# Kernel tuning notes

Hardware: AMD Instinct MI355X
Metric: run time of the kernel (lower is better)

The kernel has to match this reference:

```python
import jax, jax.numpy as jnp
import numpy as np

D_MODEL = 512
SCALE = 1.0 / (D_MODEL ** 0.5)  # module scales by 1/sqrt(d_model), not d_head
NEG = -1000000000.0

def setup_inputs() -> dict:
    key = jax.random.key(0)
    kq, kk, kv, kl = jax.random.split(key, 4)
    B, H, S, Dh = 4, 8, 2048, 64
    Q = jax.random.normal(kq, (B, H, S, Dh), dtype=jnp.float32)
    K = jax.random.normal(kk, (B, H, S, Dh), dtype=jnp.float32)
    V = jax.random.normal(kv, (B, H, S, Dh), dtype=jnp.float32)
    src_batch_lens = jax.random.randint(kl, (B,), 1, S + 1, dtype=jnp.int32)
    return {"Q": Q, "K": K, "V": V, "src_batch_lens": src_batch_lens}

def reference(Q, K, V, src_batch_lens):
    # scores: [B, H, Sq, Sk]
    scores = jnp.einsum('bhqd,bhkd->bhqk', Q, K) * SCALE
    Sk = K.shape[2]
    # mask keys at positions >= per-batch length
    key_mask = jnp.arange(Sk)[None, None, None, :] >= src_batch_lens[:, None, None, None]
    scores = jnp.where(key_mask, NEG, scores)
    attn = jax.nn.softmax(scores, axis=-1)
    # dropout is identity in eval/reference (p=0)
    context = jnp.einsum('bhqk,bhkd->bhqd', attn, V)
    return context
```

## Files before the change

kernel.cpp:

```cpp
#include <hip/hip_runtime.h>


#define S_LEN 2048
#define DH 64
#define QK_SCALE ((float)(1.4426950408889634 / 22.627416997969522))

typedef __attribute__((ext_vector_type(8))) short bf16x8;
typedef __attribute__((ext_vector_type(4))) float f32x4;

__device__ __forceinline__ short f2bf(float f) {
    __bf16 h = (__bf16)f;
    return __builtin_bit_cast(short, h);
}

#define SW(r, e) ((e) ^ (((r) & 7) << 3))

__global__ __launch_bounds__(256, 2)
void attn_fwd(const float* __restrict__ Qg, const float* __restrict__ Kg,
              const float* __restrict__ Vg, const int* __restrict__ lens,
              float* __restrict__ Og)
{
    __shared__ short Klds[2][64][64];
    __shared__ short Vt[2][64][64];

    const int tid  = threadIdx.x;
    const int wave = tid >> 6;
    const int lane = tid & 63;
    const int lr   = lane & 15;
    const int lg   = lane >> 4;

    const int bh = ((blockIdx.y & 3) << 3) | (blockIdx.y >> 2);
    const int L  = lens[bh >> 3];
    const int q0 = blockIdx.x * 64 + wave * 16;
    const size_t base = (size_t)bh * S_LEN * DH;

    bf16x8 qf[2];
    {
        const float* qrow = Qg + base + (size_t)(q0 + lr) * DH + 8 * lg;
        #pragma unroll
        for (int ks = 0; ks < 2; ++ks) {
            float4 a = *(const float4*)(qrow + 32 * ks);
            float4 b = *(const float4*)(qrow + 32 * ks + 4);
            bf16x8 f;
            f[0] = f2bf(a.x * QK_SCALE); f[1] = f2bf(a.y * QK_SCALE);
            f[2] = f2bf(a.z * QK_SCALE); f[3] = f2bf(a.w * QK_SCALE);
            f[4] = f2bf(b.x * QK_SCALE); f[5] = f2bf(b.y * QK_SCALE);
            f[6] = f2bf(b.z * QK_SCALE); f[7] = f2bf(b.w * QK_SCALE);
            qf[ks] = f;
        }
    }

    f32x4 Of[4];
    #pragma unroll
    for (int n = 0; n < 4; ++n) Of[n] = (f32x4){0.f, 0.f, 0.f, 0.f};
    f32x4 Dsum = (f32x4){0.f, 0.f, 0.f, 0.f};
    bf16x8 ones;
    #pragma unroll
    for (int j = 0; j < 8; ++j) ones[j] = (short)0x3F80;

    const int ntiles = (L + 63) >> 6;

    const int krow = tid >> 3;
    const int kc8  = (tid & 7) * 8;

    int vkey[16];
    #pragma unroll
    for (int i = 0; i < 16; ++i)
        vkey[i] = 16 * (wave & ~1) + (((i >> 2) & 1) << 4) + ((wave & 1) << 3)
                + ((i >> 3) << 2) + (i & 3);

    float4 kreg[4];
    float  vreg[16];

    {
        const float* kt = Kg + base;
        #pragma unroll
        for (int p = 0; p < 2; ++p) {
            kreg[2 * p]     = *(const float4*)(kt + (krow + 32 * p) * DH + kc8);
            kreg[2 * p + 1] = *(const float4*)(kt + (krow + 32 * p) * DH + kc8 + 4);
        }
        const float* vt = Vg + base;
        #pragma unroll
        for (int i = 0; i < 16; ++i)
            vreg[i] = vt[vkey[i] * DH + lane];
    }
    {
        #pragma unroll
        for (int p = 0; p < 2; ++p) {
            int row = krow + 32 * p;
            bf16x8 s;
            s[0] = f2bf(kreg[2*p].x); s[1] = f2bf(kreg[2*p].y);
            s[2] = f2bf(kreg[2*p].z); s[3] = f2bf(kreg[2*p].w);
            s[4] = f2bf(kreg[2*p+1].x); s[5] = f2bf(kreg[2*p+1].y);
            s[6] = f2bf(kreg[2*p+1].z); s[7] = f2bf(kreg[2*p+1].w);
            *(bf16x8*)&Klds[0][row][SW(row, kc8)] = s;
        }
        bf16x8 a, b;
        #pragma unroll
        for (int i = 0; i < 8; ++i) { a[i] = f2bf(vreg[i]); b[i] = f2bf(vreg[8 + i]); }
        *(bf16x8*)&Vt[0][lane][SW(lane, wave * 16)]     = a;
        *(bf16x8*)&Vt[0][lane][SW(lane, wave * 16 + 8)] = b;
    }
    __syncthreads();

    for (int t = 0; t < ntiles; ++t) {
        const int cur = t & 1;
        const int kb = t * 64;
        const bool pre = (t + 1 < ntiles);

        if (pre) {
            const float* kt = Kg + base + (size_t)(kb + 64) * DH;
            #pragma unroll
            for (int p = 0; p < 2; ++p) {
                kreg[2 * p]     = *(const float4*)(kt + (krow + 32 * p) * DH + kc8);
                kreg[2 * p + 1] = *(const float4*)(kt + (krow + 32 * p) * DH + kc8 + 4);
            }
            const float* vt = Vg + base + (size_t)(kb + 64) * DH;
            #pragma unroll
            for (int i = 0; i < 16; ++i)
                vreg[i] = vt[vkey[i] * DH + lane];
        }

        f32x4 Sv[4];
        #pragma unroll
        for (int n = 0; n < 4; ++n) Sv[n] = (f32x4){0.f, 0.f, 0.f, 0.f};
        #pragma unroll
        for (int ks = 0; ks < 2; ++ks) {
            #pragma unroll
            for (int n = 0; n < 4; ++n) {
                bf16x8 kf = *(const bf16x8*)&Klds[cur][16 * n + lr][SW(16 * n + lr, 8 * lg + 32 * ks)];
                Sv[n] = __builtin_amdgcn_mfma_f32_16x16x32_bf16(kf, qf[ks], Sv[n], 0, 0, 0);
            }
        }

        if (kb + 64 > L) {
            #pragma unroll
            for (int n = 0; n < 4; ++n) {
                const int kbase = kb + 16 * n + 4 * lg;
                #pragma unroll
                for (int r = 0; r < 4; ++r)
                    if (kbase + r >= L) Sv[n][r] = -1e30f;
            }
        }

        bf16x8 pf[2];
        #pragma unroll
        for (int ks = 0; ks < 2; ++ks) {
            #pragma unroll
            for (int h = 0; h < 2; ++h) {
                #pragma unroll
                for (int r = 0; r < 4; ++r)
                    pf[ks][4 * h + r] = f2bf(exp2f(Sv[2 * ks + h][r]));
            }
        }

        #pragma unroll
        for (int ks = 0; ks < 2; ++ks) {
            Dsum = __builtin_amdgcn_mfma_f32_16x16x32_bf16(pf[ks], ones, Dsum, 0, 0, 0);
            #pragma unroll
            for (int n = 0; n < 4; ++n) {
                bf16x8 vf = *(const bf16x8*)&Vt[cur][16 * n + lr][SW(16 * n + lr, 8 * lg + 32 * ks)];
                Of[n] = __builtin_amdgcn_mfma_f32_16x16x32_bf16(pf[ks], vf, Of[n], 0, 0, 0);
            }
        }

        if (pre) {
            const int b = cur ^ 1;
            #pragma unroll
            for (int p = 0; p < 2; ++p) {
                int row = krow + 32 * p;
                bf16x8 s;
                s[0] = f2bf(kreg[2*p].x); s[1] = f2bf(kreg[2*p].y);
                s[2] = f2bf(kreg[2*p].z); s[3] = f2bf(kreg[2*p].w);
                s[4] = f2bf(kreg[2*p+1].x); s[5] = f2bf(kreg[2*p+1].y);
                s[6] = f2bf(kreg[2*p+1].z); s[7] = f2bf(kreg[2*p+1].w);
                *(bf16x8*)&Klds[b][row][SW(row, kc8)] = s;
            }
            bf16x8 a, bb;
            #pragma unroll
            for (int i = 0; i < 8; ++i) { a[i] = f2bf(vreg[i]); bb[i] = f2bf(vreg[8 + i]); }
            *(bf16x8*)&Vt[b][lane][SW(lane, wave * 16)]     = a;
            *(bf16x8*)&Vt[b][lane][SW(lane, wave * 16 + 8)] = bb;
        }
        __syncthreads();
    }

    float inv[4];
    #pragma unroll
    for (int r = 0; r < 4; ++r) inv[r] = 1.f / Dsum[r];
    float* orow = Og + base + (size_t)q0 * DH;
    #pragma unroll
    for (int r = 0; r < 4; ++r) {
        int q = 4 * lg + r;
        #pragma unroll
        for (int n = 0; n < 4; ++n)
            orow[(size_t)q * DH + 16 * n + lr] = Of[n][r] * inv[r];
    }
}

extern "C" void kernel_launch(void* const* d_in, const int* in_sizes, int n_in,
                              void* d_out, int out_size, void* d_ws, size_t ws_size,
                              hipStream_t stream) {
    const float* Q = (const float*)d_in[0];
    const float* K = (const float*)d_in[1];
    const float* V = (const float*)d_in[2];
    const int* lens = (const int*)d_in[3];
    float* O = (float*)d_out;
    dim3 grid(S_LEN / 64, 4 * 8);
    attn_fwd<<<grid, 256, 0, stream>>>(Q, K, V, lens, O);
}
```

Before: 137.0 us.

## Split key range across two blocks with fp16 partials and a reduction kernel

```diff
diff --git a/kernel.cpp b/kernel.cpp
--- a/kernel.cpp
+++ b/kernel.cpp
@@ -12,13 +12,21 @@
     __bf16 h = (__bf16)f;
     return __builtin_bit_cast(short, h);
 }
+__device__ __forceinline__ short f2h(float f) {
+    _Float16 h = (_Float16)f;
+    return __builtin_bit_cast(short, h);
+}
+__device__ __forceinline__ float h2f(short s) {
+    return (float)__builtin_bit_cast(_Float16, s);
+}
 
 #define SW(r, e) ((e) ^ (((r) & 7) << 3))
 
-__global__ __launch_bounds__(256, 2)
+__global__ __launch_bounds__(512, 8)
 void attn_fwd(const float* __restrict__ Qg, const float* __restrict__ Kg,
               const float* __restrict__ Vg, const int* __restrict__ lens,
-              float* __restrict__ Og)
+              float* __restrict__ Og, short* __restrict__ pW,
+              float* __restrict__ dW, int NS)
 {
     __shared__ short Klds[2][64][64];
     __shared__ short Vt[2][64][64];
@@ -31,8 +39,14 @@
 
     const int bh = ((blockIdx.y & 3) << 3) | (blockIdx.y >> 2);
     const int L  = lens[bh >> 3];
-    const int q0 = blockIdx.x * 64 + wave * 16;
-    const size_t base = (size_t)bh * S_LEN * DH;
+    const int T  = (L + 63) >> 6;
+    const int T0 = (NS == 2) ? ((T + 1) >> 1) : T;
+    const int tb = blockIdx.z ? T0 : 0;
+    const int te = blockIdx.z ? T  : T0;
+    if (tb >= te) return;
+
+    const int q0 = blockIdx.x * 128 + wave * 16;
+    const size_t base = (size_t)bh * (S_LEN * DH);
 
     bf16x8 qf[2];
     {
@@ -58,67 +72,49 @@
     #pragma unroll
     for (int j = 0; j < 8; ++j) ones[j] = (short)0x3F80;
 
-    const int ntiles = (L + 63) >> 6;
-
     const int krow = tid >> 3;
     const int kc8  = (tid & 7) * 8;
-
-    int vkey[16];
-    #pragma unroll
-    for (int i = 0; i < 16; ++i)
-        vkey[i] = 16 * (wave & ~1) + (((i >> 2) & 1) << 4) + ((wave & 1) << 3)
-                + ((i >> 3) << 2) + (i & 3);
-
-    float4 kreg[4];
-    float  vreg[16];
+    const int vkb  = ((wave >> 2) << 5) + ((wave & 3) << 2);
+
+    float4 kreg[2];
+    float  vreg[8];
 
     {
-        const float* kt = Kg + base;
-        #pragma unroll
-        for (int p = 0; p < 2; ++p) {
-            kreg[2 * p]     = *(const float4*)(kt + (krow + 32 * p) * DH + kc8);
-            kreg[2 * p + 1] = *(const float4*)(kt + (krow + 32 * p) * DH + kc8 + 4);
-        }
-        const float* vt = Vg + base;
-        #pragma unroll
-        for (int i = 0; i < 16; ++i)
-            vreg[i] = vt[vkey[i] * DH + lane];
+        const float* kt = Kg + base + (size_t)(tb * 64) * DH;
+        kreg[0] = *(const float4*)(kt + krow * DH + kc8);
+        kreg[1] = *(const float4*)(kt + krow * DH + kc8 + 4);
+        const float* vt = Vg + base + (size_t)(tb * 64) * DH;
+        #pragma unroll
+        for (int i = 0; i < 8; ++i)
+            vreg[i] = vt[(vkb + (((i >> 2) & 1) << 4) + (i & 3)) * DH + lane];
     }
     {
-        #pragma unroll
-        for (int p = 0; p < 2; ++p) {
-            int row = krow + 32 * p;
-            bf16x8 s;
-            s[0] = f2bf(kreg[2*p].x); s[1] = f2bf(kreg[2*p].y);
-            s[2] = f2bf(kreg[2*p].z); s[3] = f2bf(kreg[2*p].w);
-            s[4] = f2bf(kreg[2*p+1].x); s[5] = f2bf(kreg[2*p+1].y);
-            s[6] = f2bf(kreg[2*p+1].z); s[7] = f2bf(kreg[2*p+1].w);
-            *(bf16x8*)&Klds[0][row][SW(row, kc8)] = s;
-        }
-        bf16x8 a, b;
-        #pragma unroll
-        for (int i = 0; i < 8; ++i) { a[i] = f2bf(vreg[i]); b[i] = f2bf(vreg[8 + i]); }
-        *(bf16x8*)&Vt[0][lane][SW(lane, wave * 16)]     = a;
-        *(bf16x8*)&Vt[0][lane][SW(lane, wave * 16 + 8)] = b;
+        bf16x8 s;
+        s[0] = f2bf(kreg[0].x); s[1] = f2bf(kreg[0].y);
+        s[2] = f2bf(kreg[0].z); s[3] = f2bf(kreg[0].w);
+        s[4] = f2bf(kreg[1].x); s[5] = f2bf(kreg[1].y);
+        s[6] = f2bf(kreg[1].z); s[7] = f2bf(kreg[1].w);
+        *(bf16x8*)&Klds[0][krow][SW(krow, kc8)] = s;
+        bf16x8 v8;
+        #pragma unroll
+        for (int i = 0; i < 8; ++i) v8[i] = f2bf(vreg[i]);
+        *(bf16x8*)&Vt[0][lane][SW(lane, 8 * wave)] = v8;
     }
     __syncthreads();
 
-    for (int t = 0; t < ntiles; ++t) {
-        const int cur = t & 1;
+    for (int t = tb; t < te; ++t) {
+        const int cur = (t - tb) & 1;
         const int kb = t * 64;
-        const bool pre = (t + 1 < ntiles);
+        const bool pre = (t + 1 < te);
 
         if (pre) {
             const float* kt = Kg + base + (size_t)(kb + 64) * DH;
-            #pragma unroll
-            for (int p = 0; p < 2; ++p) {
-                kreg[2 * p]     = *(const float4*)(kt + (krow + 32 * p) * DH + kc8);
-                kreg[2 * p + 1] = *(const float4*)(kt + (krow + 32 * p) * DH + kc8 + 4);
-            }
+            kreg[0] = *(const float4*)(kt + krow * DH + kc8);
+            kreg[1] = *(const float4*)(kt + krow * DH + kc8 + 4);
             const float* vt = Vg + base + (size_t)(kb + 64) * DH;
             #pragma unroll
-            for (int i = 0; i < 16; ++i)
-                vreg[i] = vt[vkey[i] * DH + lane];
+            for (int i = 0; i < 8; ++i)
+                vreg[i] = vt[(vkb + (((i >> 2) & 1) << 4) + (i & 3)) * DH + lane];
         }
 
         f32x4 Sv[4];
@@ -166,36 +162,71 @@
 
         if (pre) {
             const int b = cur ^ 1;
-            #pragma unroll
-            for (int p = 0; p < 2; ++p) {
-                int row = krow + 32 * p;
-                bf16x8 s;
-                s[0] = f2bf(kreg[2*p].x); s[1] = f2bf(kreg[2*p].y);
-                s[2] = f2bf(kreg[2*p].z); s[3] = f2bf(kreg[2*p].w);
-                s[4] = f2bf(kreg[2*p+1].x); s[5] = f2bf(kreg[2*p+1].y);
-                s[6] = f2bf(kreg[2*p+1].z); s[7] = f2bf(kreg[2*p+1].w);
-                *(bf16x8*)&Klds[b][row][SW(row, kc8)] = s;
-            }
-            bf16x8 a, bb;
-            #pragma unroll
-            for (int i = 0; i < 8; ++i) { a[i] = f2bf(vreg[i]); bb[i] = f2bf(vreg[8 + i]); }
-            *(bf16x8*)&Vt[b][lane][SW(lane, wave * 16)]     = a;
-            *(bf16x8*)&Vt[b][lane][SW(lane, wave * 16 + 8)] = bb;
+            bf16x8 s;
+            s[0] = f2bf(kreg[0].x); s[1] = f2bf(kreg[0].y);
+            s[2] = f2bf(kreg[0].z); s[3] = f2bf(kreg[0].w);
+            s[4] = f2bf(kreg[1].x); s[5] = f2bf(kreg[1].y);
+            s[6] = f2bf(kreg[1].z); s[7] = f2bf(kreg[1].w);
+            *(bf16x8*)&Klds[b][krow][SW(krow, kc8)] = s;
+            bf16x8 v8;
+            #pragma unroll
+            for (int i = 0; i < 8; ++i) v8[i] = f2bf(vreg[i]);
+            *(bf16x8*)&Vt[b][lane][SW(lane, 8 * wave)] = v8;
         }
         __syncthreads();
     }
 
-    float inv[4];
-    #pragma unroll
-    for (int r = 0; r < 4; ++r) inv[r] = 1.f / Dsum[r];
-    float* orow = Og + base + (size_t)q0 * DH;
-    #pragma unroll
-    for (int r = 0; r < 4; ++r) {
-        int q = 4 * lg + r;
-        #pragma unroll
-        for (int n = 0; n < 4; ++n)
-            orow[(size_t)q * DH + 16 * n + lr] = Of[n][r] * inv[r];
-    }
+    if (NS == 1) {
+        float inv[4];
+        #pragma unroll
+        for (int r = 0; r < 4; ++r) inv[r] = 1.f / Dsum[r];
+        float* orow = Og + base + (size_t)q0 * DH;
+        #pragma unroll
+        for (int r = 0; r < 4; ++r) {
+            int q = 4 * lg + r;
+            #pragma unroll
+            for (int n = 0; n < 4; ++n)
+                orow[(size_t)q * DH + 16 * n + lr] = Of[n][r] * inv[r];
+        }
+    } else {
+        short* prow = pW + ((size_t)(blockIdx.z * 32 + bh) * S_LEN + q0) * DH;
+        #pragma unroll
+        for (int r = 0; r < 4; ++r) {
+            int q = 4 * lg + r;
+            #pragma unroll
+            for (int n = 0; n < 4; ++n)
+                prow[(size_t)q * DH + 16 * n + lr] = f2h(Of[n][r]);
+        }
+        if (lr == 0) {
+            #pragma unroll
+            for (int r = 0; r < 4; ++r)
+                dW[(size_t)(blockIdx.z * 32 + bh) * S_LEN + q0 + 4 * lg + r] = Dsum[r];
+        }
+    }
+}
+
+__global__ __launch_bounds__(256)
+void attn_reduce(const int* __restrict__ lens, const short* __restrict__ pW,
+                 const float* __restrict__ dW, float* __restrict__ Og)
+{
+    const size_t i = ((size_t)blockIdx.x * 256 + threadIdx.x) * 4;
+    const int bh = (int)(i >> 17);
+    const int q  = (int)((i >> 6) & (S_LEN - 1));
+    const int L  = lens[bh >> 3];
+    const int T  = (L + 63) >> 6;
+    const int T0 = (T + 1) >> 1;
+    const int nact = (T > T0) ? 2 : 1;
+
+    float ax = 0.f, ay = 0.f, az = 0.f, aw = 0.f, den = 0.f;
+    for (int s = 0; s < nact; ++s) {
+        const size_t sb = (size_t)(s * 32 + bh);
+        short4 h = *(const short4*)(pW + sb * ((size_t)S_LEN * DH) + (i & ((size_t)S_LEN * DH - 1)));
+        ax += h2f(h.x); ay += h2f(h.y); az += h2f(h.z); aw += h2f(h.w);
+        den += dW[sb * S_LEN + q];
+    }
+    const float inv = 1.f / den;
+    float4 o; o.x = ax * inv; o.y = ay * inv; o.z = az * inv; o.w = aw * inv;
+    *(float4*)(Og + i) = o;
 }
 
 extern "C" void kernel_launch(void* const* d_in, const int* in_sizes, int n_in,
@@ -206,6 +237,17 @@
     const float* V = (const float*)d_in[2];
     const int* lens = (const int*)d_in[3];
     float* O = (float*)d_out;
-    dim3 grid(S_LEN / 64, 4 * 8);
-    attn_fwd<<<grid, 256, 0, stream>>>(Q, K, V, lens, O);
-}
+
+    const size_t outN = (size_t)4 * 8 * S_LEN * DH;
+    const size_t need2 = 2 * outN * 2 + (size_t)2 * 32 * S_LEN * 4;
+    const int NS = (ws_size >= need2) ? 2 : 1;
+
+    short* pW = (short*)d_ws;
+    float* dW = (float*)((char*)d_ws + (size_t)NS * outN * 2);
+
+    dim3 grid(S_LEN / 128, 32, NS);
+    attn_fwd<<<grid, 512, 0, stream>>>(Q, K, V, lens, O, pW, dW, NS);
+    if (NS == 2) {
+        attn_reduce<<<(unsigned)(outN / 1024), 256, 0, stream>>>(lens, pW, dW, O);
+    }
+}
```

Measured after the change: 230.4 us. 68.1% more time.
